# Optimization experiments

Measured on AMD Instinct MI355X. Metric: run time of the kernel, lower is better.

The kernel has to match this reference:

```python
import jax, jax.numpy as jnp
import numpy as np

EPS = 1e-5
LEAK = 0.33  # scn LeakyReLU default leakiness


def leaky(x):
    return jnp.where(x > 0, x, LEAK * x)


def subm_conv(feat, idx, mask, w):
    # feat: [N,C], idx: [N,K] int, mask: [N,K] bool, w: [K,Cin,Cout]
    g = feat[idx] * mask[..., None]          # [N,K,C] gather of active neighbors
    return jnp.einsum('nkc,kcd->nd', g, w)   # [N,Cout]


def batch_norm(x, gamma, beta):
    # scn BatchNormalization in training mode: batch stats over active sites
    m = x.mean(axis=0)
    v = x.var(axis=0)
    return (x - m) * jax.lax.rsqrt(v + EPS) * gamma + beta


def setup_inputs() -> dict:
    key = jax.random.key(0)
    ks = jax.random.split(key, 8)
    N, K, C, B = 131072, 9, 64, 4
    features = jax.random.normal(ks[0], (N, C), dtype=jnp.float32)
    neighbor_idx = jax.random.randint(ks[1], (N, K), 0, N, dtype=jnp.int32)
    # center offset always points at self (submanifold conv semantics)
    neighbor_idx = neighbor_idx.at[:, K // 2].set(jnp.arange(N, dtype=jnp.int32))
    neighbor_mask = jax.random.randint(ks[2], (N, K), 0, 2) > 0
    neighbor_mask = neighbor_mask.at[:, K // 2].set(True)
    scale = 1.0 / np.sqrt(K * C)
    conv1_w = jax.random.normal(ks[3], (B, K, C, C), dtype=jnp.float32) * scale
    conv2_w = jax.random.normal(ks[4], (B, K, C, C), dtype=jnp.float32) * scale
    bn1_gamma = jnp.ones((B, C), dtype=jnp.float32)
    bn1_beta = jnp.zeros((B, C), dtype=jnp.float32)
    bn2_gamma = jnp.ones((B, C), dtype=jnp.float32)
    bn2_beta = jnp.zeros((B, C), dtype=jnp.float32)
    return {
        'features': features, 'neighbor_idx': neighbor_idx, 'neighbor_mask': neighbor_mask,
        'conv1_w': conv1_w, 'bn1_gamma': bn1_gamma, 'bn1_beta': bn1_beta,
        'conv2_w': conv2_w, 'bn2_gamma': bn2_gamma, 'bn2_beta': bn2_beta,
    }


def reference(features, neighbor_idx, neighbor_mask, conv1_w, bn1_gamma, bn1_beta,
              conv2_w, bn2_gamma, bn2_beta):
    x = features
    n_blocks = conv1_w.shape[0]
    for b in range(n_blocks):
        residual = x
        out = subm_conv(x, neighbor_idx, neighbor_mask, conv1_w[b])
        out = leaky(batch_norm(out, bn1_gamma[b], bn1_beta[b]))
        out = subm_conv(out, neighbor_idx, neighbor_mask, conv2_w[b])
        out = batch_norm(out, bn2_gamma[b], bn2_beta[b])
        x = leaky(out + residual)
    return x
```

## Files before the change

### kernel.cpp

```cpp
#include <hip/hip_runtime.h>
#include <hip/hip_bf16.h>
#include <stdint.h>

#define NROWS 131072
#define EPSBN 1e-5f
#define LEAKK 0.33f

typedef __bf16 bf16x8_t __attribute__((ext_vector_type(8)));
typedef float  f32x4_t  __attribute__((ext_vector_type(4)));

__device__ __forceinline__ float leaky_f(float x) { return fmaxf(x, LEAKK * x); }

#define GLDS16(g, l)                                                          \
    __builtin_amdgcn_global_load_lds(                                         \
        (const __attribute__((address_space(1))) void*)(g),                   \
        (__attribute__((address_space(3))) void*)(l), 16, 0, 0)

#define WAIT_VM18  0x4F72
#define WAIT_VM10  0x0F7A
#define WAIT_VM8   0x0F78
#define WAIT_VM0   0x0F70
#define WAIT_LGKM0 0xC07F
#define CFENCE() asm volatile("" ::: "memory")

__global__ __launch_bounds__(256, 2) void conv_kernel(
    const __bf16* __restrict__ src,
    const int* __restrict__ cidxT,
    const __bf16* __restrict__ wt,
    __bf16* __restrict__ dst,
    float* __restrict__ stat_out)
{
    __shared__ char Ab[2][32768];
    __shared__ char Bb[2][8192];

    const int tid  = threadIdx.x;
    const int lane = tid & 63;
    const int wv   = tid >> 6;
    const int quad = lane >> 4;
    const int l15  = lane & 15;
    const int row0 = blockIdx.x << 8;
    const int srow = tid >> 3;
    const int cg   = (tid & 7) ^ (srow & 7);
    const int ldsl = (tid & 192) << 4;
    const int sxor = l15 & 7;

    const char* srcb = (const char*)src;
    const char* wtb  = (const char*)wt;

    f32x4_t acc[4][4];
#pragma unroll
    for (int mt = 0; mt < 4; ++mt)
#pragma unroll
        for (int nt = 0; nt < 4; ++nt)
            acc[mt][nt] = (f32x4_t){0.f, 0.f, 0.f, 0.f};

    int ix[2][8];
#pragma unroll
    for (int i = 0; i < 8; ++i) ix[0][i] = cidxT[row0 + (i << 5) + srow];
    CFENCE();
#pragma unroll
    for (int i = 0; i < 8; ++i) ix[1][i] = cidxT[NROWS + row0 + (i << 5) + srow];
    CFENCE();
    __builtin_amdgcn_s_waitcnt(WAIT_VM8);
#pragma unroll
    for (int i = 0; i < 8; ++i)
        GLDS16(srcb + ((size_t)ix[0][i] << 7) + (cg << 4), &Ab[0][(i << 12) + ldsl]);
#pragma unroll
    for (int i = 0; i < 2; ++i)
        GLDS16(wtb + (((i << 5) + srow) << 7) + (cg << 4), &Bb[0][(i << 12) + ldsl]);
    CFENCE();

#pragma unroll
    for (int k = 0; k < 9; ++k) {
        const int cur = k & 1, nxt = cur ^ 1;
        if (k < 7) {
#pragma unroll
            for (int i = 0; i < 8; ++i)
                ix[k & 1][i] = cidxT[(k + 2) * NROWS + row0 + (i << 5) + srow];
        }
        CFENCE();
        if (k < 8) {
            const int* ixu = ix[(k + 1) & 1];
#pragma unroll
            for (int i = 0; i < 8; ++i)
                GLDS16(srcb + ((size_t)ixu[i] << 7) + (cg << 4),
                       &Ab[nxt][(i << 12) + ldsl]);
#pragma unroll
            for (int i = 0; i < 2; ++i)
                GLDS16(wtb + ((size_t)(k + 1) << 13) + (((i << 5) + srow) << 7) + (cg << 4),
                       &Bb[nxt][(i << 12) + ldsl]);
        }
        CFENCE();
        if (k < 7)       __builtin_amdgcn_s_waitcnt(WAIT_VM18);
        else if (k == 7) __builtin_amdgcn_s_waitcnt(WAIT_VM10);
        else             __builtin_amdgcn_s_waitcnt(WAIT_VM0);
        __builtin_amdgcn_s_barrier();
        bf16x8_t af[4][2], bq[4][2];
#pragma unroll
        for (int ks = 0; ks < 2; ++ks) {
            const int slot = ((quad | (ks << 2)) ^ sxor) << 4;
#pragma unroll
            for (int mt = 0; mt < 4; ++mt) {
                int m = (wv << 6) + (mt << 4) + l15;
                af[mt][ks] = *(const bf16x8_t*)&Ab[cur][(m << 7) + slot];
            }
#pragma unroll
            for (int nt = 0; nt < 4; ++nt) {
                int d = (nt << 4) + l15;
                bq[nt][ks] = *(const bf16x8_t*)&Bb[cur][(d << 7) + slot];
            }
        }
#pragma unroll
        for (int ks = 0; ks < 2; ++ks)
#pragma unroll
            for (int mt = 0; mt < 4; ++mt)
#pragma unroll
                for (int nt = 0; nt < 4; ++nt)
                    acc[mt][nt] = __builtin_amdgcn_mfma_f32_16x16x32_bf16(
                        af[mt][ks], bq[nt][ks], acc[mt][nt], 0, 0, 0);
        CFENCE();
        __builtin_amdgcn_s_waitcnt(WAIT_LGKM0);
        __builtin_amdgcn_s_barrier();
        CFENCE();
    }

#pragma unroll
    for (int mt = 0; mt < 4; ++mt) {
        int rowb = row0 + (wv << 6) + (mt << 4) + (quad << 2);
#pragma unroll
        for (int nt = 0; nt < 4; ++nt) {
            int col = (nt << 4) + l15;
#pragma unroll
            for (int r = 0; r < 4; ++r)
                dst[((size_t)(rowb + r) << 6) + col] = (__bf16)acc[mt][nt][r];
        }
    }
    float* red = (float*)Bb[1];
    __syncthreads();
    if (tid < 128) red[tid] = 0.f;
    __syncthreads();
#pragma unroll
    for (int nt = 0; nt < 4; ++nt) {
        float s = 0.f, q = 0.f;
#pragma unroll
        for (int mt = 0; mt < 4; ++mt)
#pragma unroll
            for (int r = 0; r < 4; ++r) { float v = acc[mt][nt][r]; s += v; q += v * v; }
        s += __shfl_xor(s, 16); s += __shfl_xor(s, 32);
        q += __shfl_xor(q, 16); q += __shfl_xor(q, 32);
        if (lane < 16) {
            atomicAdd(&red[(nt << 4) + lane], s);
            atomicAdd(&red[64 + (nt << 4) + lane], q);
        }
    }
    __syncthreads();
    if (tid < 128) atomicAdd(&stat_out[tid], red[tid]);
}

__global__ __launch_bounds__(256) void bnact_kernel(
    __bf16* __restrict__ y, const float* __restrict__ stat,
    const float* __restrict__ gamma, const float* __restrict__ beta)
{
    __shared__ float sc[64], sh[64];
    int tid = threadIdx.x;
    if (tid < 64) {
        float m = stat[tid] * (1.f / NROWS);
        float v = stat[64 + tid] * (1.f / NROWS) - m * m;
        float s = gamma[tid] * rsqrtf(v + EPSBN);
        sc[tid] = s;
        sh[tid] = beta[tid] - m * s;
    }
    __syncthreads();
    size_t base = ((((size_t)blockIdx.x << 8) | tid) << 3);
    int c0 = (int)(base & 63);
    bf16x8_t hv = *(bf16x8_t*)(y + base);
#pragma unroll
    for (int j = 0; j < 8; ++j) {
        float f = (float)hv[j];
        f = leaky_f(f * sc[c0 + j] + sh[c0 + j]);
        hv[j] = (__bf16)f;
    }
    *(bf16x8_t*)(y + base) = hv;
}

__global__ __launch_bounds__(256) void resid_kernel(
    const __bf16* __restrict__ z, const float* __restrict__ featin,
    __bf16* __restrict__ xh, float* __restrict__ dout,
    const float* __restrict__ stat, const float* __restrict__ gamma,
    const float* __restrict__ beta, int isfirst, int isfinal)
{
    __shared__ float sc[64], sh[64];
    int tid = threadIdx.x;
    if (tid < 64) {
        float m = stat[tid] * (1.f / NROWS);
        float v = stat[64 + tid] * (1.f / NROWS) - m * m;
        float s = gamma[tid] * rsqrtf(v + EPSBN);
        sc[tid] = s;
        sh[tid] = beta[tid] - m * s;
    }
    __syncthreads();
    size_t base = ((((size_t)blockIdx.x << 8) | tid) << 3);
    int c0 = (int)(base & 63);
    bf16x8_t zv = *(const bf16x8_t*)(z + base);
    float xv[8];
    if (isfirst) {
        float4 xa = *(const float4*)(featin + base);
        float4 xb = *(const float4*)(featin + base + 4);
#pragma unroll
        for (int j = 0; j < 4; ++j) { xv[j] = (&xa.x)[j]; xv[4 + j] = (&xb.x)[j]; }
    } else {
        bf16x8_t xr = *(const bf16x8_t*)(xh + base);
#pragma unroll
        for (int j = 0; j < 8; ++j) xv[j] = (float)xr[j];
    }
    float o[8];
#pragma unroll
    for (int j = 0; j < 8; ++j)
        o[j] = leaky_f((float)zv[j] * sc[c0 + j] + sh[c0 + j] + xv[j]);
    if (isfinal) {
        *(float4*)(dout + base)     = make_float4(o[0], o[1], o[2], o[3]);
        *(float4*)(dout + base + 4) = make_float4(o[4], o[5], o[6], o[7]);
    } else {
        bf16x8_t h;
#pragma unroll
        for (int j = 0; j < 8; ++j) h[j] = (__bf16)o[j];
        *(bf16x8_t*)(xh + base) = h;
    }
}

__global__ __launch_bounds__(256) void prep_kernel(
    const float* __restrict__ feat, const float* __restrict__ w1,
    const float* __restrict__ w2, const int* __restrict__ nidx,
    const unsigned char* __restrict__ mraw,
    __bf16* __restrict__ fh, __bf16* __restrict__ yh,
    __bf16* __restrict__ wtp, int* __restrict__ cidxT,
    float* __restrict__ stats)
{
    size_t t = ((size_t)blockIdx.x << 8) | threadIdx.x;
    if (t < 1024) stats[t] = 0.f;
    if (t < 64) {
        fh[(size_t)NROWS * 64 + t] = (__bf16)0.f;
        yh[(size_t)NROWS * 64 + t] = (__bf16)0.f;
    }
    if (t < 1048576) {
        size_t i = t << 3;
        float4 a = *(const float4*)(feat + i);
        float4 b = *(const float4*)(feat + i + 4);
        bf16x8_t h;
        h[0] = (__bf16)a.x; h[1] = (__bf16)a.y; h[2] = (__bf16)a.z; h[3] = (__bf16)a.w;
        h[4] = (__bf16)b.x; h[5] = (__bf16)b.y; h[6] = (__bf16)b.z; h[7] = (__bf16)b.w;
        *(bf16x8_t*)(fh + i) = h;
    }
    if (t < 294912) {
        int o = (int)t;
        int c = o & 63, d = (o >> 6) & 63;
        int kk = o >> 12;
        int k = kk % 9, bb = (kk / 9) & 3, cv = kk / 36;
        const float* w = cv ? w2 : w1;
        float v = w[((size_t)((bb * 9 + k) * 64 + c) << 6) + d];
        wtp[o] = (__bf16)v;
    }
    if (t < NROWS) {
        int n = (int)t;
        bool benc = (mraw[13] != 0);
        const unsigned int* mw = (const unsigned int*)mraw;
#pragma unroll
        for (int j = 0; j < 9; ++j) {
            int e = n * 9 + j;
            bool m = benc ? (mraw[e] != 0) : (mw[e] != 0u);
            cidxT[j * NROWS + n] = m ? nidx[e] : NROWS;
        }
    }
}

extern "C" void kernel_launch(void* const* d_in, const int* in_sizes, int n_in,
                              void* d_out, int out_size, void* d_ws, size_t ws_size,
                              hipStream_t stream) {
    const float* feat = (const float*)d_in[0];
    const int* nidx = (const int*)d_in[1];
    const unsigned char* mraw = (const unsigned char*)d_in[2];
    const float* w1 = (const float*)d_in[3];
    const float* g1 = (const float*)d_in[4];
    const float* b1 = (const float*)d_in[5];
    const float* w2 = (const float*)d_in[6];
    const float* g2 = (const float*)d_in[7];
    const float* b2 = (const float*)d_in[8];
    float* out = (float*)d_out;

    char* ws = (char*)d_ws;
    __bf16* xh    = (__bf16*)ws;
    __bf16* yh    = (__bf16*)(ws + 17825792);
    __bf16* zh    = (__bf16*)(ws + 35651584);
    __bf16* wtp   = (__bf16*)(ws + 53477376);
    float*  stats = (float*)(ws + 54525952);
    int*    cidxT = (int*)(ws + 54591488);

    prep_kernel<<<4096, 256, 0, stream>>>(feat, w1, w2, nidx, mraw,
                                          xh, yh, wtp, cidxT, stats);

    for (int b = 0; b < 4; ++b) {
        conv_kernel<<<512, 256, 0, stream>>>(
            xh, cidxT, wtp + (size_t)b * 9 * 4096,
            yh, stats + (size_t)(2 * b) * 128);
        bnact_kernel<<<4096, 256, 0, stream>>>(
            yh, stats + (size_t)(2 * b) * 128, g1 + b * 64, b1 + b * 64);
        conv_kernel<<<512, 256, 0, stream>>>(
            yh, cidxT, wtp + (size_t)(4 + b) * 9 * 4096,
            zh, stats + (size_t)(2 * b + 1) * 128);
        resid_kernel<<<4096, 256, 0, stream>>>(
            zh, feat, xh, out,
            stats + (size_t)(2 * b + 1) * 128, g2 + b * 64, b2 + b * 64,
            (b == 0) ? 1 : 0, (b == 3) ? 1 : 0);
    }
}
```

Before: 400.3 us.

## Load gathered A fragments directly to registers and preload all weights into LDS

The conv kernel stops staging the gathered neighbour rows through double-buffered LDS and has each lane load its MFMA A-fragments straight from global memory into registers, double-buffered across the 9 offsets. All 9 weight slices are loaded into LDS once up front, so the per-iteration barriers and hand-tuned waitcnts go away. This removes LDS traffic and block-wide synchronisation per offset. In exchange the gathers become per-lane 16-byte loads with less coalescing, register pressure rises, and LDS usage grows to 72KB, which may limit occupancy.

```diff
diff --git a/kernel.cpp b/kernel.cpp
--- a/kernel.cpp
+++ b/kernel.cpp
@@ -16,11 +16,6 @@
         (const __attribute__((address_space(1))) void*)(g),                   \
         (__attribute__((address_space(3))) void*)(l), 16, 0, 0)
 
-#define WAIT_VM18  0x4F72
-#define WAIT_VM10  0x0F7A
-#define WAIT_VM8   0x0F78
-#define WAIT_VM0   0x0F70
-#define WAIT_LGKM0 0xC07F
 #define CFENCE() asm volatile("" ::: "memory")
 
 __global__ __launch_bounds__(256, 2) void conv_kernel(
@@ -30,8 +25,7 @@
     __bf16* __restrict__ dst,
     float* __restrict__ stat_out)
 {
-    __shared__ char Ab[2][32768];
-    __shared__ char Bb[2][8192];
+    __shared__ char Bw[9][8192];
 
     const int tid  = threadIdx.x;
     const int lane = tid & 63;
@@ -54,61 +48,62 @@
         for (int nt = 0; nt < 4; ++nt)
             acc[mt][nt] = (f32x4_t){0.f, 0.f, 0.f, 0.f};
 
-    int ix[2][8];
-#pragma unroll
-    for (int i = 0; i < 8; ++i) ix[0][i] = cidxT[row0 + (i << 5) + srow];
+    const int ibase = row0 + (wv << 6) + l15;
+    const unsigned qofs = (unsigned)(quad << 4);
+
+    int ixv[2][4];
+#pragma unroll
+    for (int mt = 0; mt < 4; ++mt) ixv[0][mt] = cidxT[ibase + (mt << 4)];
+#pragma unroll
+    for (int mt = 0; mt < 4; ++mt) ixv[1][mt] = cidxT[NROWS + ibase + (mt << 4)];
     CFENCE();
 #pragma unroll
-    for (int i = 0; i < 8; ++i) ix[1][i] = cidxT[NROWS + row0 + (i << 5) + srow];
+    for (int k = 0; k < 9; ++k)
+#pragma unroll
+        for (int i = 0; i < 2; ++i)
+            GLDS16(wtb + (k << 13) + (((i << 5) + srow) << 7) + (cg << 4),
+                   &Bw[k][(i << 12) + ldsl]);
     CFENCE();
-    __builtin_amdgcn_s_waitcnt(WAIT_VM8);
-#pragma unroll
-    for (int i = 0; i < 8; ++i)
-        GLDS16(srcb + ((size_t)ix[0][i] << 7) + (cg << 4), &Ab[0][(i << 12) + ldsl]);
-#pragma unroll
-    for (int i = 0; i < 2; ++i)
-        GLDS16(wtb + (((i << 5) + srow) << 7) + (cg << 4), &Bb[0][(i << 12) + ldsl]);
+    asm volatile("s_waitcnt vmcnt(0)" ::: "memory");
+    __builtin_amdgcn_s_barrier();
     CFENCE();
 
+    bf16x8_t areg[2][4][2];
+#pragma unroll
+    for (int mt = 0; mt < 4; ++mt) {
+        unsigned vo = ((unsigned)ixv[0][mt] << 7) + qofs;
+#pragma unroll
+        for (int ks = 0; ks < 2; ++ks)
+            areg[0][mt][ks] = *(const bf16x8_t*)(srcb + vo + (ks << 6));
+    }
+    CFENCE();
+
 #pragma unroll
     for (int k = 0; k < 9; ++k) {
-        const int cur = k & 1, nxt = cur ^ 1;
         if (k < 7) {
 #pragma unroll
-            for (int i = 0; i < 8; ++i)
-                ix[k & 1][i] = cidxT[(k + 2) * NROWS + row0 + (i << 5) + srow];
+            for (int mt = 0; mt < 4; ++mt)
+                ixv[k & 1][mt] = cidxT[(k + 2) * NROWS + ibase + (mt << 4)];
+        }
+        if (k < 8) {
+#pragma unroll
+            for (int mt = 0; mt < 4; ++mt) {
+                unsigned vo = ((unsigned)ixv[(k + 1) & 1][mt] << 7) + qofs;
+#pragma unroll
+                for (int ks = 0; ks < 2; ++ks)
+                    areg[(k + 1) & 1][mt][ks] =
+                        *(const bf16x8_t*)(srcb + vo + (ks << 6));
+            }
         }
         CFENCE();
-        if (k < 8) {
-            const int* ixu = ix[(k + 1) & 1];
-#pragma unroll
-            for (int i = 0; i < 8; ++i)
-                GLDS16(srcb + ((size_t)ixu[i] << 7) + (cg << 4),
-                       &Ab[nxt][(i << 12) + ldsl]);
-#pragma unroll
-            for (int i = 0; i < 2; ++i)
-                GLDS16(wtb + ((size_t)(k + 1) << 13) + (((i << 5) + srow) << 7) + (cg << 4),
-                       &Bb[nxt][(i << 12) + ldsl]);
-        }
-        CFENCE();
-        if (k < 7)       __builtin_amdgcn_s_waitcnt(WAIT_VM18);
-        else if (k == 7) __builtin_amdgcn_s_waitcnt(WAIT_VM10);
-        else             __builtin_amdgcn_s_waitcnt(WAIT_VM0);
-        __builtin_amdgcn_s_barrier();
-        bf16x8_t af[4][2], bq[4][2];
+        bf16x8_t bq[4][2];
 #pragma unroll
         for (int ks = 0; ks < 2; ++ks) {
             const int slot = ((quad | (ks << 2)) ^ sxor) << 4;
 #pragma unroll
-            for (int mt = 0; mt < 4; ++mt) {
-                int m = (wv << 6) + (mt << 4) + l15;
-                af[mt][ks] = *(const bf16x8_t*)&Ab[cur][(m << 7) + slot];
-            }
-#pragma unroll
-            for (int nt = 0; nt < 4; ++nt) {
-                int d = (nt << 4) + l15;
-                bq[nt][ks] = *(const bf16x8_t*)&Bb[cur][(d << 7) + slot];
-            }
+            for (int nt = 0; nt < 4; ++nt)
+                bq[nt][ks] = *(const bf16x8_t*)
+                    &Bw[k][(((nt << 4) + l15) << 7) + slot];
         }
 #pragma unroll
         for (int ks = 0; ks < 2; ++ks)
@@ -117,10 +112,7 @@
 #pragma unroll
                 for (int nt = 0; nt < 4; ++nt)
                     acc[mt][nt] = __builtin_amdgcn_mfma_f32_16x16x32_bf16(
-                        af[mt][ks], bq[nt][ks], acc[mt][nt], 0, 0, 0);
-        CFENCE();
-        __builtin_amdgcn_s_waitcnt(WAIT_LGKM0);
-        __builtin_amdgcn_s_barrier();
+                        areg[k & 1][mt][ks], bq[nt][ks], acc[mt][nt], 0, 0, 0);
         CFENCE();
     }
 
@@ -135,7 +127,7 @@
                 dst[((size_t)(rowb + r) << 6) + col] = (__bf16)acc[mt][nt][r];
         }
     }
-    float* red = (float*)Bb[1];
+    float* red = (float*)Bw;
     __syncthreads();
     if (tid < 128) red[tid] = 0.f;
     __syncthreads();
```

New measurement: 404.2 us. About the same (+1.0%).
